# Performance work log

Measured on AMD Instinct MI355X. Metric: run time of the kernel, lower is better.

Reference implementation:

```python
import jax, jax.numpy as jnp
import numpy as np

B, S, D = 4, 2048, 2048
H, DH = 16, 128


def setup_inputs() -> dict:
    key = jax.random.key(0)
    k1, k2, k3, k4, k5 = jax.random.split(key, 5)
    x = jax.random.normal(k1, (B, S, D), dtype=jnp.float32)
    # causal mask, broadcast over heads and batch (module does mask.unsqueeze(0))
    attn_mask = jnp.tril(jnp.ones((S, S), dtype=jnp.int32))
    # torch Linear weights: [out, in]; scaled like default init
    w_qkv = jax.random.normal(k2, (3 * H * DH, D), dtype=jnp.float32) / np.sqrt(D)
    b_qkv = jax.random.normal(k3, (3 * H * DH,), dtype=jnp.float32) * 0.01
    w_out = jax.random.normal(k4, (D, H * DH), dtype=jnp.float32) / np.sqrt(H * DH)
    b_out = jax.random.normal(k5, (D,), dtype=jnp.float32) * 0.01
    return {"x": x, "attn_mask": attn_mask, "w_qkv": w_qkv, "b_qkv": b_qkv,
            "w_out": w_out, "b_out": b_out}


def reference(x, attn_mask, w_qkv, b_qkv, w_out, b_out):
    b, s, d = x.shape
    qkv = x @ w_qkv.T + b_qkv                      # [B,S,3*H*DH]
    qkv = qkv.reshape(b, s, H, 3 * DH)             # per-head contiguous 3*DH slice
    qkv = jnp.transpose(qkv, (2, 0, 1, 3))         # [H,B,S,3*DH]
    q, k, v = jnp.split(qkv, 3, axis=-1)           # each [H,B,S,DH]
    scores = jnp.einsum('hbqd,hbkd->hbqk', q, k) / np.sqrt(DH)
    scores = jnp.where(attn_mask[None, None] == 0, -jnp.inf, scores)
    attn = jax.nn.softmax(scores, axis=-1)         # dropout is identity at eval
    ctx = jnp.einsum('hbqk,hbkd->hbqd', attn, v)   # [H,B,S,DH]
    ctx = jnp.transpose(ctx, (1, 2, 0, 3)).reshape(b, s, H * DH)
    return ctx @ w_out.T + b_out
```

## Files before the change

### kernel.cpp

```cpp
#include <hip/hip_runtime.h>

typedef unsigned short u16;
typedef __bf16 bf16x8 __attribute__((ext_vector_type(8)));
typedef unsigned short u16x8 __attribute__((ext_vector_type(8)));
typedef float f32x4 __attribute__((ext_vector_type(4)));

#define GLDS16(gp, lp)                                                        \
  __builtin_amdgcn_global_load_lds(                                           \
      (const __attribute__((address_space(1))) void*)(gp),                    \
      (__attribute__((address_space(3))) void*)(lp), 16, 0, 0)

__device__ __forceinline__ u16 f2bf(float f) {
  unsigned u = __float_as_uint(f);
  u += 0x7FFFu + ((u >> 16) & 1u);
  return (u16)(u >> 16);
}

__device__ __forceinline__ f32x4 mfma_bf16(bf16x8 a, bf16x8 b, f32x4 c) {
  return __builtin_amdgcn_mfma_f32_16x16x32_bf16(a, b, c, 0, 0, 0);
}

__global__ void cvt_f32_bf16(const float* __restrict__ src,
                             u16* __restrict__ dst, int n8) {
  for (int i = blockIdx.x * blockDim.x + threadIdx.x; i < n8;
       i += gridDim.x * blockDim.x) {
    const float4* sp = (const float4*)src + (size_t)i * 2;
    float4 a = sp[0], b = sp[1];
    u16x8 o;
    o[0] = f2bf(a.x); o[1] = f2bf(a.y); o[2] = f2bf(a.z); o[3] = f2bf(a.w);
    o[4] = f2bf(b.x); o[5] = f2bf(b.y); o[6] = f2bf(b.z); o[7] = f2bf(b.w);
    *((u16x8*)dst + i) = o;
  }
}

template <int OUT_BF16>
__global__ __launch_bounds__(256) void gemm_bt(const u16* __restrict__ A,
                                               const u16* __restrict__ B,
                                               const float* __restrict__ bias,
                                               void* __restrict__ Cout, int M,
                                               int N, int K) {
  __shared__ __attribute__((aligned(16))) u16 As[128 * 64];
  __shared__ __attribute__((aligned(16))) u16 Bs[128 * 64];
  const int t = threadIdx.x, lane = t & 63, w = t >> 6;
  const int l15 = lane & 15, l4 = lane >> 4;
  const int bm = blockIdx.x * 128, bn = blockIdx.y * 128;
  const int wr = (w >> 1) * 64, wc = (w & 1) * 64;

  f32x4 z4 = {0.f, 0.f, 0.f, 0.f};
  f32x4 acc[4][4];
#pragma unroll
  for (int i = 0; i < 4; ++i)
#pragma unroll
    for (int j = 0; j < 4; ++j) acc[i][j] = z4;

  const int srow = t >> 3;
  const int scol = ((t & 7) ^ (srow & 7)) << 3;
  const u16* Ag = A + (size_t)(bm + srow) * K + scol;
  const u16* Bg = B + (size_t)(bn + srow) * K + scol;
  u16* AsW = As + w * 512;
  u16* BsW = Bs + w * 512;

  for (int k0 = 0; k0 < K; k0 += 64) {
    __syncthreads();
#pragma unroll
    for (int i = 0; i < 4; ++i) {
      GLDS16(Ag + k0 + i * 32 * K, AsW + i * 2048);
      GLDS16(Bg + k0 + i * 32 * K, BsW + i * 2048);
    }
    __syncthreads();
#pragma unroll
    for (int kc = 0; kc < 2; ++kc) {
      bf16x8 af[4], bf[4];
#pragma unroll
      for (int x = 0; x < 4; ++x) {
        int ra = wr + x * 16 + l15;
        af[x] = *(const bf16x8*)(As + ra * 64 + (((kc * 4 + l4) ^ (ra & 7)) << 3));
        int rb = wc + x * 16 + l15;
        bf[x] = *(const bf16x8*)(Bs + rb * 64 + (((kc * 4 + l4) ^ (rb & 7)) << 3));
      }
#pragma unroll
      for (int mi = 0; mi < 4; ++mi)
#pragma unroll
        for (int ni = 0; ni < 4; ++ni)
          acc[mi][ni] = mfma_bf16(af[mi], bf[ni], acc[mi][ni]);
    }
  }
  const int cr = l4 * 4, cc = l15;
#pragma unroll
  for (int ni = 0; ni < 4; ++ni) {
    int col = bn + wc + ni * 16 + cc;
    float bv = bias[col];
#pragma unroll
    for (int mi = 0; mi < 4; ++mi)
#pragma unroll
      for (int r = 0; r < 4; ++r) {
        int row = bm + wr + mi * 16 + cr + r;
        float v = acc[mi][ni][r] + bv;
        if (OUT_BF16)
          ((u16*)Cout)[(size_t)row * N + col] = f2bf(v);
        else
          ((float*)Cout)[(size_t)row * N + col] = v;
      }
  }
}

__device__ __forceinline__ int vt_idx(int d, int kk) {
  int swz = (d ^ (d >> 3)) & 7;
  return d * 64 + ((((kk >> 3) ^ swz) << 3) | (kk & 7));
}
__device__ __forceinline__ int ps_idx(int r, int c) {
  return r * 64 + ((((c >> 3) ^ ((r >> 2) & 7)) << 3) | (c & 7));
}

__global__ __launch_bounds__(256, 2) void attn_fwd(const u16* __restrict__ qkv,
                                                   u16* __restrict__ ctx) {
  constexpr int NQ = 6144, SD = 2048;
  __shared__ __attribute__((aligned(16))) u16 Ks[2][64 * 128];
  __shared__ __attribute__((aligned(16))) u16 Vt[2][128 * 64];
  __shared__ __attribute__((aligned(16))) u16 Ps[128 * 64];
  const int t = threadIdx.x, lane = t & 63, w = t >> 6;
  const int l15 = lane & 15, l4 = lane >> 4;
  const int h = blockIdx.y, b = blockIdx.z;
  const size_t rowbase = (size_t)b * 2048;
  const int hq = h * 384;

  const u16* Kg = qkv + (rowbase + (t >> 4)) * NQ + hq + 128 +
                  (((t & 15) ^ ((t >> 4) & 7)) << 3);
  const u16* Vg = qkv + (rowbase + (t & 15)) * NQ + hq + 256 + ((t >> 4) << 3);
  const int vkk = t & 15, vd0 = (t >> 4) << 3;

  const float C = 0.12751879522447905f;
  const float THRC = 62.73592239488341f;

  for (int seg = 0; seg < 2; ++seg) {
    const int qt = (seg == 0) ? (15 - (int)blockIdx.x) : (int)blockIdx.x;
    const int q0 = qt * 128;
    const int nt = 2 * qt + 2;
    const int qr0 = q0 + w * 32 + l4 * 4;

    bf16x8 qf[2][4];
#pragma unroll
    for (int mi = 0; mi < 2; ++mi) {
      const u16* qp =
          qkv + (rowbase + q0 + w * 32 + mi * 16 + l15) * NQ + hq + l4 * 8;
#pragma unroll
      for (int kc = 0; kc < 4; ++kc) qf[mi][kc] = *(const bf16x8*)(qp + kc * 32);
    }

    f32x4 z4 = {0.f, 0.f, 0.f, 0.f};
    f32x4 oacc[2][8];
#pragma unroll
    for (int mi = 0; mi < 2; ++mi)
#pragma unroll
      for (int i = 0; i < 8; ++i) oacc[mi][i] = z4;
    float m_run[2][4], l_run[2][4];
#pragma unroll
    for (int mi = 0; mi < 2; ++mi)
#pragma unroll
      for (int r = 0; r < 4; ++r) { m_run[mi][r] = -3.0e38f; l_run[mi][r] = 0.f; }

    u16x8 vA[4], vB[4];
#pragma unroll
    for (int i = 0; i < 4; ++i)
      GLDS16(Kg + (size_t)(i * 16) * NQ, &Ks[0][i * 2048 + w * 512]);
#pragma unroll
    for (int p = 0; p < 4; ++p)
      vA[p] = *(const u16x8*)(Vg + (size_t)(p * 16) * NQ);
    __syncthreads();
#pragma unroll
    for (int p = 0; p < 4; ++p) {
      int kk = p * 16 + vkk;
#pragma unroll
      for (int j = 0; j < 8; ++j) Vt[0][vt_idx(vd0 + j, kk)] = vA[p][j];
    }
#pragma unroll
    for (int p = 0; p < 4; ++p)
      vA[p] = *(const u16x8*)(Vg + (size_t)(64 + p * 16) * NQ);
    __syncthreads();

    for (int tt = 0; tt < nt; ++tt) {
      const int k0 = tt * 64, cur = tt & 1;
      const int kn = (k0 + 64 < q0 + 64) ? k0 + 64 : q0 + 64;
#pragma unroll
      for (int i = 0; i < 4; ++i)
        GLDS16(Kg + (size_t)(kn + i * 16) * NQ,
               &Ks[cur ^ 1][i * 2048 + w * 512]);
      const int kv = (k0 + 128 < q0 + 64) ? k0 + 128 : q0 + 64;
#pragma unroll
      for (int p = 0; p < 4; ++p)
        vB[p] = *(const u16x8*)(Vg + (size_t)(kv + p * 16) * NQ);

      f32x4 sc[2][4];
#pragma unroll
      for (int mi = 0; mi < 2; ++mi)
#pragma unroll
        for (int nf = 0; nf < 4; ++nf) sc[mi][nf] = z4;
#pragma unroll
      for (int kc = 0; kc < 4; ++kc)
#pragma unroll
        for (int nf = 0; nf < 4; ++nf) {
          int rk = nf * 16 + l15;
          bf16x8 kf = *(const bf16x8*)(&Ks[cur][rk * 128 +
                                              (((kc * 4 + l4) ^ (rk & 7)) << 3)]);
          sc[0][nf] = mfma_bf16(qf[0][kc], kf, sc[0][nf]);
          sc[1][nf] = mfma_bf16(qf[1][kc], kf, sc[1][nf]);
        }
      if (tt + 2 >= nt) {
#pragma unroll
        for (int mi = 0; mi < 2; ++mi)
#pragma unroll
          for (int nf = 0; nf < 4; ++nf) {
            int col = k0 + nf * 16 + l15;
            int qr = qr0 + mi * 16;
#pragma unroll
            for (int r = 0; r < 4; ++r)
              if (col > qr + r) sc[mi][nf][r] = -3.0e38f;
          }
      }
      float mx[2][4];
#pragma unroll
      for (int mi = 0; mi < 2; ++mi)
#pragma unroll
        for (int r = 0; r < 4; ++r)
          mx[mi][r] = fmaxf(fmaxf(sc[mi][0][r], sc[mi][1][r]),
                            fmaxf(sc[mi][2][r], sc[mi][3][r]));
#pragma unroll
      for (int off = 8; off >= 1; off >>= 1)
#pragma unroll
        for (int mi = 0; mi < 2; ++mi)
#pragma unroll
          for (int r = 0; r < 4; ++r)
            mx[mi][r] = fmaxf(mx[mi][r], __shfl_xor(mx[mi][r], off));
      bool upd = false;
#pragma unroll
      for (int mi = 0; mi < 2; ++mi)
#pragma unroll
        for (int r = 0; r < 4; ++r)
          upd |= (mx[mi][r] > m_run[mi][r] + THRC);
      if (__any(upd)) {
#pragma unroll
        for (int mi = 0; mi < 2; ++mi)
#pragma unroll
          for (int r = 0; r < 4; ++r) {
            float mn = fmaxf(m_run[mi][r], mx[mi][r]);
            float cr = exp2f((m_run[mi][r] - mn) * C);
            m_run[mi][r] = mn;
            l_run[mi][r] *= cr;
#pragma unroll
            for (int nf = 0; nf < 8; ++nf) oacc[mi][nf][r] *= cr;
          }
      }
#pragma unroll
      for (int mi = 0; mi < 2; ++mi) {
        float mC[4], sm[4];
#pragma unroll
        for (int r = 0; r < 4; ++r) mC[r] = m_run[mi][r] * C;
#pragma unroll
        for (int nf = 0; nf < 4; ++nf)
#pragma unroll
          for (int r = 0; r < 4; ++r)
            sc[mi][nf][r] = exp2f(fmaf(sc[mi][nf][r], C, -mC[r]));
#pragma unroll
        for (int r = 0; r < 4; ++r)
          sm[r] = (sc[mi][0][r] + sc[mi][1][r]) + (sc[mi][2][r] + sc[mi][3][r]);
#pragma unroll
        for (int off = 8; off >= 1; off >>= 1)
#pragma unroll
          for (int r = 0; r < 4; ++r) sm[r] += __shfl_xor(sm[r], off);
#pragma unroll
        for (int r = 0; r < 4; ++r) l_run[mi][r] += sm[r];
#pragma unroll
        for (int nf = 0; nf < 4; ++nf)
#pragma unroll
          for (int r = 0; r < 4; ++r)
            ((__bf16*)Ps)[ps_idx(w * 32 + mi * 16 + l4 * 4 + r,
                                 nf * 16 + l15)] = (__bf16)sc[mi][nf][r];
      }
#pragma unroll
      for (int p = 0; p < 4; ++p) {
        int kk = p * 16 + vkk;
#pragma unroll
        for (int j = 0; j < 8; ++j) Vt[cur ^ 1][vt_idx(vd0 + j, kk)] = vA[p][j];
      }
#pragma unroll
      for (int kc = 0; kc < 2; ++kc) {
        bf16x8 pf0 =
            *(const bf16x8*)(Ps + ps_idx(w * 32 + l15, kc * 32 + l4 * 8));
        bf16x8 pf1 =
            *(const bf16x8*)(Ps + ps_idx(w * 32 + 16 + l15, kc * 32 + l4 * 8));
#pragma unroll
        for (int nf = 0; nf < 8; ++nf) {
          bf16x8 vf = *(const bf16x8*)(&Vt[cur][vt_idx(nf * 16 + l15,
                                                       kc * 32 + l4 * 8)]);
          oacc[0][nf] = mfma_bf16(pf0, vf, oacc[0][nf]);
          oacc[1][nf] = mfma_bf16(pf1, vf, oacc[1][nf]);
        }
      }
      __syncthreads();
#pragma unroll
      for (int p = 0; p < 4; ++p) vA[p] = vB[p];
    }
#pragma unroll
    for (int mi = 0; mi < 2; ++mi) {
      float inv[4];
#pragma unroll
      for (int r = 0; r < 4; ++r) inv[r] = 1.f / l_run[mi][r];
      u16* cp = ctx + (rowbase + q0 + w * 32 + mi * 16 + l4 * 4) * SD +
                h * 128 + l15;
#pragma unroll
      for (int nf = 0; nf < 8; ++nf)
#pragma unroll
        for (int r = 0; r < 4; ++r)
          ((__bf16*)cp)[(size_t)r * SD + nf * 16] =
              (__bf16)(oacc[mi][nf][r] * inv[r]);
    }
  }
}

extern "C" void kernel_launch(void* const* d_in, const int* in_sizes, int n_in,
                              void* d_out, int out_size, void* d_ws,
                              size_t ws_size, hipStream_t stream) {
  const float* x = (const float*)d_in[0];
  const float* wqkv = (const float*)d_in[2];
  const float* bqkv = (const float*)d_in[3];
  const float* wout = (const float*)d_in[4];
  const float* bout = (const float*)d_in[5];
  float* out = (float*)d_out;
  char* ws = (char*)d_ws;

  u16* xb = (u16*)(ws);
  u16* wqkvb = (u16*)(ws + 33554432);
  u16* woutb = (u16*)(ws + 58720256);
  u16* qkvb = (u16*)(ws + 67108864);
  u16* ctx = xb;

  cvt_f32_bf16<<<2048, 256, 0, stream>>>(x, xb, 16777216 / 8);
  cvt_f32_bf16<<<2048, 256, 0, stream>>>(wqkv, wqkvb, 12582912 / 8);
  cvt_f32_bf16<<<1024, 256, 0, stream>>>(wout, woutb, 4194304 / 8);
  gemm_bt<1><<<dim3(64, 48), 256, 0, stream>>>(xb, wqkvb, bqkv, qkvb, 8192,
                                               6144, 2048);
  attn_fwd<<<dim3(8, 16, 4), 256, 0, stream>>>(qkvb, ctx);
  gemm_bt<0><<<dim3(64, 16), 256, 0, stream>>>(ctx, woutb, bout, out, 8192,
                                               2048, 2048);
}
```

Before: 688.4 us.

## Replace GEMM with 256x256 8-wave ping-pong pipelined kernel and XCD-swizzled grid

Replaces the 128x128 single-buffered GEMM with a 256x256-tile, 512-thread kernel that double-buffers A/B halves in LDS, interleaves global-to-LDS staging with MFMA phases under fine-grained barriers and explicit vmcnt waits, and remaps block IDs across XCDs for L2 locality. It also raises wave priority around MFMA loops in both the GEMM and the attention kernel. The aim is to hide global load latency and increase data reuse per tile. The trade-off is much higher register and LDS pressure (128 KB LDS, 32 accumulators per thread) and a hand-ordered wait count that is fragile.

```diff
diff --git a/kernel.cpp b/kernel.cpp
--- a/kernel.cpp
+++ b/kernel.cpp
@@ -34,73 +34,140 @@
 }
 
 template <int OUT_BF16>
-__global__ __launch_bounds__(256) void gemm_bt(const u16* __restrict__ A,
-                                               const u16* __restrict__ B,
-                                               const float* __restrict__ bias,
-                                               void* __restrict__ Cout, int M,
-                                               int N, int K) {
-  __shared__ __attribute__((aligned(16))) u16 As[128 * 64];
-  __shared__ __attribute__((aligned(16))) u16 Bs[128 * 64];
+__global__ __launch_bounds__(512, 2) void gemm8p(const u16* __restrict__ A,
+                                                 const u16* __restrict__ B,
+                                                 const float* __restrict__ bias,
+                                                 void* __restrict__ Cout,
+                                                 int M, int N, int K, int nbm) {
+  __shared__ __attribute__((aligned(16))) u16 L[2][4][8192];
   const int t = threadIdx.x, lane = t & 63, w = t >> 6;
   const int l15 = lane & 15, l4 = lane >> 4;
-  const int bm = blockIdx.x * 128, bn = blockIdx.y * 128;
-  const int wr = (w >> 1) * 64, wc = (w & 1) * 64;
-
+  const int wm = w >> 2, wn = w & 3;
+
+  const int cpx = (int)gridDim.x >> 3;
+  const int wg = (int)blockIdx.x;
+  const int swz = (wg & 7) * cpx + (wg >> 3);
+  const int bm = (swz % nbm) * 256;
+  const int bn = (swz / nbm) * 256;
+
+  const size_t aoff = (size_t)(t >> 3) * K + (((t & 7) ^ ((t >> 3) & 7)) << 3);
+  const u16* SB[4] = {A + (size_t)bm * K, A + (size_t)(bm + 128) * K,
+                      B + (size_t)bn * K, B + (size_t)(bn + 128) * K};
+  const int ldst = w << 9;
+
+#define STG(d, s, l, kt)                                                      \
+  GLDS16(SB[s] + (size_t)(l) * 64 * K + (size_t)(kt) * 64 + aoff,             \
+         &L[d][s][(l) * 4096 + ldst])
+#define BAR __builtin_amdgcn_s_barrier()
+#define WAITL asm volatile("s_waitcnt lgkmcnt(0)" ::: "memory")
+
+  f32x4 acc[8][4];
   f32x4 z4 = {0.f, 0.f, 0.f, 0.f};
-  f32x4 acc[4][4];
-#pragma unroll
-  for (int i = 0; i < 4; ++i)
+#pragma unroll
+  for (int i = 0; i < 8; ++i)
 #pragma unroll
     for (int j = 0; j < 4; ++j) acc[i][j] = z4;
 
-  const int srow = t >> 3;
-  const int scol = ((t & 7) ^ (srow & 7)) << 3;
-  const u16* Ag = A + (size_t)(bm + srow) * K + scol;
-  const u16* Bg = B + (size_t)(bn + srow) * K + scol;
-  u16* AsW = As + w * 512;
-  u16* BsW = Bs + w * 512;
-
-  for (int k0 = 0; k0 < K; k0 += 64) {
-    __syncthreads();
-#pragma unroll
-    for (int i = 0; i < 4; ++i) {
-      GLDS16(Ag + k0 + i * 32 * K, AsW + i * 2048);
-      GLDS16(Bg + k0 + i * 32 * K, BsW + i * 2048);
-    }
-    __syncthreads();
-#pragma unroll
-    for (int kc = 0; kc < 2; ++kc) {
-      bf16x8 af[4], bf[4];
-#pragma unroll
-      for (int x = 0; x < 4; ++x) {
-        int ra = wr + x * 16 + l15;
-        af[x] = *(const bf16x8*)(As + ra * 64 + (((kc * 4 + l4) ^ (ra & 7)) << 3));
-        int rb = wc + x * 16 + l15;
-        bf[x] = *(const bf16x8*)(Bs + rb * 64 + (((kc * 4 + l4) ^ (rb & 7)) << 3));
-      }
-#pragma unroll
-      for (int mi = 0; mi < 4; ++mi)
-#pragma unroll
-        for (int ni = 0; ni < 4; ++ni)
-          acc[mi][ni] = mfma_bf16(af[mi], bf[ni], acc[mi][ni]);
-    }
+  const u16* AH[2] = {&L[0][wm][0], &L[1][wm][0]};
+  const u16* BH[2] = {&L[0][2 + (wn >> 1)][0], &L[1][2 + (wn >> 1)][0]};
+  const int cb = (wn & 1) * 64;
+
+  bf16x8 af[4][2], bfr[4][2];
+
+  auto rdA = [&](const u16* H, int mh) {
+#pragma unroll
+    for (int m2 = 0; m2 < 4; ++m2) {
+      int ra = mh * 64 + m2 * 16 + l15;
+      const u16* p = H + ra * 64;
+      af[m2][0] = *(const bf16x8*)(p + ((l4 ^ (ra & 7)) << 3));
+      af[m2][1] = *(const bf16x8*)(p + (((4 + l4) ^ (ra & 7)) << 3));
+    }
+  };
+  auto rdB = [&](const u16* H, int nh) {
+#pragma unroll
+    for (int n2 = 0; n2 < 2; ++n2) {
+      int rb = cb + (nh * 2 + n2) * 16 + l15;
+      const u16* p = H + rb * 64;
+      bfr[nh * 2 + n2][0] = *(const bf16x8*)(p + ((l4 ^ (rb & 7)) << 3));
+      bfr[nh * 2 + n2][1] = *(const bf16x8*)(p + (((4 + l4) ^ (rb & 7)) << 3));
+    }
+  };
+  auto mma = [&](int mh, int nh) {
+    __builtin_amdgcn_s_setprio(1);
+#pragma unroll
+    for (int m2 = 0; m2 < 4; ++m2)
+#pragma unroll
+      for (int n2 = 0; n2 < 2; ++n2) {
+        int ai = mh * 4 + m2, bi = nh * 2 + n2;
+        acc[ai][bi] = mfma_bf16(af[m2][0], bfr[bi][0], acc[ai][bi]);
+        acc[ai][bi] = mfma_bf16(af[m2][1], bfr[bi][1], acc[ai][bi]);
+      }
+    __builtin_amdgcn_s_setprio(0);
+  };
+
+  STG(0, 0, 0, 0); STG(0, 0, 1, 0); STG(0, 1, 0, 0); STG(0, 1, 1, 0);
+  STG(0, 2, 0, 0); STG(0, 2, 1, 0); STG(0, 3, 0, 0); STG(0, 3, 1, 0);
+  STG(1, 0, 0, 1); STG(1, 1, 0, 1); STG(1, 2, 0, 1); STG(1, 2, 1, 1);
+  STG(1, 3, 0, 1); STG(1, 3, 1, 1);
+  asm volatile("s_waitcnt vmcnt(0)" ::: "memory");
+  BAR;
+
+  const int NI = K >> 7;
+  for (int i = 0; i < NI; ++i) {
+    const int kt = 2 * i;
+    const bool st = (i + 1 < NI);
+    rdA(AH[0], 0); rdB(BH[0], 0);
+    STG(1, 0, 1, kt + 1); STG(1, 1, 1, kt + 1);
+    BAR; WAITL; mma(0, 0); BAR;
+    rdB(BH[0], 1);
+    if (st) { STG(0, 0, 0, kt + 2); STG(0, 1, 0, kt + 2); }
+    BAR; WAITL; mma(0, 1); BAR;
+    rdA(AH[0], 1);
+    if (st) { STG(0, 2, 0, kt + 2); STG(0, 2, 1, kt + 2); }
+    BAR; WAITL; mma(1, 1); BAR;
+    if (st) {
+      STG(0, 3, 0, kt + 2); STG(0, 3, 1, kt + 2);
+      asm volatile("s_waitcnt vmcnt(6)" ::: "memory");
+    } else {
+      asm volatile("s_waitcnt vmcnt(0)" ::: "memory");
+    }
+    BAR; mma(1, 0); BAR;
+    rdA(AH[1], 0); rdB(BH[1], 0);
+    if (st) { STG(0, 0, 1, kt + 2); STG(0, 1, 1, kt + 2); }
+    BAR; WAITL; mma(0, 0); BAR;
+    rdB(BH[1], 1);
+    if (st) { STG(1, 0, 0, kt + 3); STG(1, 1, 0, kt + 3); }
+    BAR; WAITL; mma(0, 1); BAR;
+    rdA(AH[1], 1);
+    if (st) { STG(1, 2, 0, kt + 3); STG(1, 2, 1, kt + 3); }
+    BAR; WAITL; mma(1, 1); BAR;
+    if (st) {
+      STG(1, 3, 0, kt + 3); STG(1, 3, 1, kt + 3);
+      asm volatile("s_waitcnt vmcnt(6)" ::: "memory");
+    }
+    BAR; mma(1, 0); BAR;
   }
-  const int cr = l4 * 4, cc = l15;
+#undef STG
+#undef BAR
+#undef WAITL
+
+  const int cr = l4 * 4;
 #pragma unroll
   for (int ni = 0; ni < 4; ++ni) {
-    int col = bn + wc + ni * 16 + cc;
+    int col = bn + wn * 64 + ni * 16 + l15;
     float bv = bias[col];
 #pragma unroll
-    for (int mi = 0; mi < 4; ++mi)
+    for (int mi = 0; mi < 8; ++mi) {
+      int row = bm + wm * 128 + mi * 16 + cr;
 #pragma unroll
       for (int r = 0; r < 4; ++r) {
-        int row = bm + wr + mi * 16 + cr + r;
         float v = acc[mi][ni][r] + bv;
         if (OUT_BF16)
-          ((u16*)Cout)[(size_t)row * N + col] = f2bf(v);
+          ((u16*)Cout)[(size_t)(row + r) * N + col] = f2bf(v);
         else
-          ((float*)Cout)[(size_t)row * N + col] = v;
-      }
+          ((float*)Cout)[(size_t)(row + r) * N + col] = v;
+      }
+    }
   }
 }
 
@@ -195,6 +262,7 @@
       for (int mi = 0; mi < 2; ++mi)
 #pragma unroll
         for (int nf = 0; nf < 4; ++nf) sc[mi][nf] = z4;
+      __builtin_amdgcn_s_setprio(1);
 #pragma unroll
       for (int kc = 0; kc < 4; ++kc)
 #pragma unroll
@@ -205,6 +273,7 @@
           sc[0][nf] = mfma_bf16(qf[0][kc], kf, sc[0][nf]);
           sc[1][nf] = mfma_bf16(qf[1][kc], kf, sc[1][nf]);
         }
+      __builtin_amdgcn_s_setprio(0);
       if (tt + 2 >= nt) {
 #pragma unroll
         for (int mi = 0; mi < 2; ++mi)
@@ -288,6 +357,7 @@
             *(const bf16x8*)(Ps + ps_idx(w * 32 + l15, kc * 32 + l4 * 8));
         bf16x8 pf1 =
             *(const bf16x8*)(Ps + ps_idx(w * 32 + 16 + l15, kc * 32 + l4 * 8));
+        __builtin_amdgcn_s_setprio(1);
 #pragma unroll
         for (int nf = 0; nf < 8; ++nf) {
           bf16x8 vf = *(const bf16x8*)(&Vt[cur][vt_idx(nf * 16 + l15,
@@ -295,6 +365,7 @@
           oacc[0][nf] = mfma_bf16(pf0, vf, oacc[0][nf]);
           oacc[1][nf] = mfma_bf16(pf1, vf, oacc[1][nf]);
         }
+        __builtin_amdgcn_s_setprio(0);
       }
       __syncthreads();
 #pragma unroll
@@ -337,9 +408,9 @@
   cvt_f32_bf16<<<2048, 256, 0, stream>>>(x, xb, 16777216 / 8);
   cvt_f32_bf16<<<2048, 256, 0, stream>>>(wqkv, wqkvb, 12582912 / 8);
   cvt_f32_bf16<<<1024, 256, 0, stream>>>(wout, woutb, 4194304 / 8);
-  gemm_bt<1><<<dim3(64, 48), 256, 0, stream>>>(xb, wqkvb, bqkv, qkvb, 8192,
-                                               6144, 2048);
+  gemm8p<1><<<dim3(32 * 24), 512, 0, stream>>>(xb, wqkvb, bqkv, qkvb, 8192,
+                                               6144, 2048, 32);
   attn_fwd<<<dim3(8, 16, 4), 256, 0, stream>>>(qkvb, ctx);
-  gemm_bt<0><<<dim3(64, 16), 256, 0, stream>>>(ctx, woutb, bout, out, 8192,
-                                               2048, 2048);
-}
+  gemm8p<0><<<dim3(32 * 8), 512, 0, stream>>>(ctx, woutb, bout, out, 8192,
+                                              2048, 2048, 32);
+}
```

Result: slower. 753.8 us (+9.5%).
